# Kernel tuning notes

Measured on AMD Instinct MI355X. Metric: run time of the kernel, lower is better.

Reference implementation:

```python
import jax, jax.numpy as jnp
import numpy as np

N = 50000
E = 800000
IN = 256
H = 4
C = 64
HC = H * C
LAT = 64
EPS = 1e-5
NEG_SLOPE = 0.2


def setup_inputs() -> dict:
    key = jax.random.key(0)
    ks = jax.random.split(key, 20)
    g = lambda k, shape, fan: jax.random.normal(k, shape, jnp.float32) * (1.0 / np.sqrt(fan))
    return {
        "x": jax.random.normal(ks[0], (N, IN), jnp.float32),
        "edge_index": jax.random.randint(ks[1], (2, E), 0, N, jnp.int32),
        "Wl1": g(ks[2], (IN, HC), IN), "Wr1": g(ks[3], (IN, HC), IN),
        "att1": g(ks[4], (H, C), C), "b1": jnp.zeros((HC,), jnp.float32),
        "ln1_g": jnp.ones((HC,), jnp.float32), "ln1_b": jnp.zeros((HC,), jnp.float32),
        "Wl2": g(ks[5], (HC, HC), HC), "Wr2": g(ks[6], (HC, HC), HC),
        "att2": g(ks[7], (H, C), C), "b2": jnp.zeros((HC,), jnp.float32),
        "ln2_g": jnp.ones((HC,), jnp.float32), "ln2_b": jnp.zeros((HC,), jnp.float32),
        "Wmu": g(ks[8], (HC, LAT), HC), "bmu": jnp.zeros((LAT,), jnp.float32),
        "Wlv": g(ks[9], (HC, LAT), HC), "blv": jnp.zeros((LAT,), jnp.float32),
    }


def _gatv2_layer(x, src, dst, Wl, Wr, att, bias):
    # GATv2: e_ij = att . leaky_relu(Wl x_j + Wr x_i); segment softmax over dst; aggregate Wl x_j
    xl = (x @ Wl).reshape(-1, H, C)  # source transform [N,H,C]
    xr = (x @ Wr).reshape(-1, H, C)  # target transform [N,H,C]
    e = jax.nn.leaky_relu(xl[src] + xr[dst], NEG_SLOPE)   # [E',H,C]
    score = jnp.einsum('ehc,hc->eh', e, att)              # [E',H]
    m = jax.ops.segment_max(score, dst, num_segments=N)   # [N,H]
    ex = jnp.exp(score - m[dst])
    denom = jax.ops.segment_sum(ex, dst, num_segments=N)  # [N,H]
    alpha = ex / denom[dst]                               # self-loops guarantee denom > 0
    out = jax.ops.segment_sum(alpha[:, :, None] * xl[src], dst, num_segments=N)  # [N,H,C]
    return out.reshape(-1, HC) + bias


def _layernorm(x, g, b):
    mu = jnp.mean(x, axis=-1, keepdims=True)
    var = jnp.mean((x - mu) ** 2, axis=-1, keepdims=True)
    return (x - mu) * jax.lax.rsqrt(var + EPS) * g + b


def reference(x, edge_index, Wl1, Wr1, att1, b1, ln1_g, ln1_b,
              Wl2, Wr2, att2, b2, ln2_g, ln2_b, Wmu, bmu, Wlv, blv):
    loops = jnp.arange(N, dtype=edge_index.dtype)
    src = jnp.concatenate([edge_index[0], loops])  # add_self_loops=True
    dst = jnp.concatenate([edge_index[1], loops])
    h = _gatv2_layer(x, src, dst, Wl1, Wr1, att1, b1)
    h = jax.nn.elu(_layernorm(h, ln1_g, ln1_b))  # dropout is identity in eval mode
    h = _gatv2_layer(h, src, dst, Wl2, Wr2, att2, b2)
    h = jax.nn.elu(_layernorm(h, ln2_g, ln2_b))
    mu = h @ Wmu + bmu
    logvar = h @ Wlv + blv
    return mu, logvar
```

## Files before the change

### kernel.cpp

```cpp
#include <hip/hip_runtime.h>
#include <hip/hip_bf16.h>

#define NN 50000
#define NE 800000
#define HCn 256
#define LATn 64

typedef short bf16x4 __attribute__((ext_vector_type(4)));
typedef short bf16x8 __attribute__((ext_vector_type(8)));
typedef float f32x4 __attribute__((ext_vector_type(4)));

__device__ __forceinline__ short f2b(float f) {
    __hip_bfloat16 h = __float2bfloat16(f);
    return __builtin_bit_cast(short, h);
}
__device__ __forceinline__ float b2f(short s) {
    return __bfloat162float(__builtin_bit_cast(__hip_bfloat16, s));
}

#define SWZF(v, pat) __builtin_bit_cast(float, __builtin_amdgcn_ds_swizzle(__builtin_bit_cast(int, v), pat))

#define C04L2E 0.5770780163555854f
#define C06L2E 0.8656170245333781f
#define DEFER_THR 8.0f

__global__ void hist_kernel(const int* __restrict__ dst, int* __restrict__ counts) {
    int e = blockIdx.x * 256 + threadIdx.x;
    if (e < NE) atomicAdd(&counts[dst[e]], 1);
}

__global__ __launch_bounds__(1024) void scan1_kernel(int* __restrict__ counts,
                                                     int* __restrict__ blocksum) {
    const int g = blockIdx.x * 1024 + threadIdx.x;
    const int lane = threadIdx.x & 63;
    const int wv = threadIdx.x >> 6;
    int v = (g < NN) ? counts[g] : 0;
    int s = v;
#pragma unroll
    for (int d = 1; d < 64; d <<= 1) {
        int t = __shfl_up(s, d, 64);
        if (lane >= d) s += t;
    }
    __shared__ int wsum[16];
    if (lane == 63) wsum[wv] = s;
    __syncthreads();
    if (threadIdx.x == 0) {
        int run = 0;
#pragma unroll
        for (int q = 0; q < 16; ++q) { int t = wsum[q]; wsum[q] = run; run += t; }
        blocksum[blockIdx.x] = run;
    }
    __syncthreads();
    int excl = s - v + wsum[wv];
    if (g < NN) counts[g] = excl;
}

__global__ void scan2_kernel(int* __restrict__ blocksum, int* __restrict__ offsets, int nblk) {
    const int lane = threadIdx.x;
    int v = (lane < nblk) ? blocksum[lane] : 0;
    int s = v;
#pragma unroll
    for (int d = 1; d < 64; d <<= 1) {
        int t = __shfl_up(s, d, 64);
        if (lane >= d) s += t;
    }
    if (lane < nblk) blocksum[lane] = s - v;
    if (lane == 0) offsets[NN] = NE;
}

__global__ __launch_bounds__(1024) void scan3_kernel(const int* __restrict__ counts,
                                                     const int* __restrict__ blocksum,
                                                     int* __restrict__ offsets,
                                                     int* __restrict__ cursor) {
    const int g = blockIdx.x * 1024 + threadIdx.x;
    if (g < NN) {
        int v = counts[g] + blocksum[blockIdx.x];
        offsets[g] = v;
        cursor[g]  = v;
    }
}

__global__ void scatter_kernel(const int* __restrict__ src, const int* __restrict__ dst,
                               int* __restrict__ cursor, int* __restrict__ csr_src) {
    int e = blockIdx.x * 256 + threadIdx.x;
    if (e < NE) {
        int p = atomicAdd(&cursor[dst[e]], 1);
        csr_src[p] = src[e];
    }
}

__global__ __launch_bounds__(256) void cvt_x_kernel(const float* __restrict__ x,
                                                    short* __restrict__ xb) {
    long i = ((long)blockIdx.x * 256 + threadIdx.x) * 8;
    const f32x4* p = reinterpret_cast<const f32x4*>(x + i);
    f32x4 a = p[0], b = p[1];
    bf16x8 o;
#pragma unroll
    for (int j = 0; j < 4; ++j) { o[j] = f2b(a[j]); o[4 + j] = f2b(b[j]); }
    *reinterpret_cast<bf16x8*>(xb + i) = o;
}

__global__ void pack_w_kernel(const float* __restrict__ Wl1, const float* __restrict__ Wr1,
                              const float* __restrict__ Wl2, const float* __restrict__ Wr2,
                              const float* __restrict__ Wmu, const float* __restrict__ Wlv,
                              const float* __restrict__ bmu, const float* __restrict__ blv,
                              short* __restrict__ Wb1t, short* __restrict__ Wb2t,
                              short* __restrict__ Wb3t, float* __restrict__ bias3) {
    int i = blockIdx.x * 256 + threadIdx.x;
    const int S1 = 512 * 256, S2 = 2 * S1, S3 = S2 + 128 * 256;
    if (i < S1) {
        int c = i >> 8, k = i & 255;
        float v = (c < 256) ? Wl1[k * 256 + c] : Wr1[k * 256 + (c - 256)];
        Wb1t[i] = f2b(v);
    } else if (i < S2) {
        int j = i - S1; int c = j >> 8, k = j & 255;
        float v = (c < 256) ? Wl2[k * 256 + c] : Wr2[k * 256 + (c - 256)];
        Wb2t[j] = f2b(v);
    } else if (i < S3) {
        int j = i - S2; int c = j >> 8, k = j & 255;
        float v = (c < 64) ? Wmu[k * 64 + c] : Wlv[k * 64 + (c - 64)];
        Wb3t[j] = f2b(v);
    } else if (i < S3 + 128) {
        int c = i - S3;
        bias3[c] = (c < 64) ? bmu[c] : blv[c - 64];
    }
}

template<int OUT_MODE>
__global__ __launch_bounds__(256) void gemm_k(
    const short* __restrict__ A, const short* __restrict__ Wbt,
    void* __restrict__ outp, const float* __restrict__ bias, int Nc)
{
    __shared__ short Bs[64 * 264];
    const int t = threadIdx.x;
    const int w = t >> 6, lane = t & 63;
    const int row0 = blockIdx.x * 128, col0 = blockIdx.y * 64;

    {
        const int sn = t >> 2;
        const int sk0 = (t & 3) * 8;
        const short* wp = Wbt + (long)(col0 + sn) * 256 + sk0;
#pragma unroll
        for (int r = 0; r < 8; ++r) {
            int k = r * 32 + sk0;
            bf16x8 v = *reinterpret_cast<const bf16x8*>(wp + r * 32);
            *reinterpret_cast<bf16x8*>(&Bs[sn * 264 + k]) = v;
        }
    }
    __syncthreads();

    f32x4 acc[2][4];
#pragma unroll
    for (int a = 0; a < 2; ++a)
#pragma unroll
        for (int b = 0; b < 4; ++b) acc[a][b] = (f32x4){0.f, 0.f, 0.f, 0.f};

    const int arow = lane & 15, kq = lane >> 4;
    int r0 = row0 + w * 32 + arow;      if (r0 > NN - 1) r0 = NN - 1;
    int r1 = row0 + w * 32 + 16 + arow; if (r1 > NN - 1) r1 = NN - 1;
    const short* pa0 = A + (long)r0 * 256 + kq * 8;
    const short* pa1 = A + (long)r1 * 256 + kq * 8;

#pragma unroll
    for (int k0 = 0; k0 < 256; k0 += 32) {
        bf16x8 a0 = *reinterpret_cast<const bf16x8*>(pa0 + k0);
        bf16x8 a1 = *reinterpret_cast<const bf16x8*>(pa1 + k0);
#pragma unroll
        for (int nt = 0; nt < 4; ++nt) {
            bf16x8 b = *reinterpret_cast<const bf16x8*>(&Bs[(nt * 16 + arow) * 264 + k0 + kq * 8]);
            acc[0][nt] = __builtin_amdgcn_mfma_f32_16x16x32_bf16(a0, b, acc[0][nt], 0, 0, 0);
            acc[1][nt] = __builtin_amdgcn_mfma_f32_16x16x32_bf16(a1, b, acc[1][nt], 0, 0, 0);
        }
    }

#pragma unroll
    for (int rb = 0; rb < 2; ++rb)
#pragma unroll
        for (int nt = 0; nt < 4; ++nt) {
            int gcol = col0 + nt * 16 + arow;
#pragma unroll
            for (int r = 0; r < 4; ++r) {
                int grow = row0 + w * 32 + rb * 16 + kq * 4 + r;
                if (grow < NN) {
                    float v = acc[rb][nt][r];
                    if (OUT_MODE == 0) {
                        ((short*)outp)[(long)grow * Nc + gcol] = f2b(v);
                    } else {
                        v += bias[gcol];
                        float* o = (float*)outp;
                        if (gcol < 64) o[(long)grow * 64 + gcol] = v;
                        else           o[(long)NN * 64 + (long)grow * 64 + (gcol - 64)] = v;
                    }
                }
            }
        }
}

__global__ __launch_bounds__(256) void att_pre_kernel(
    const short* __restrict__ xlr, const float* __restrict__ att, float* __restrict__ a)
{
    const int i = blockIdx.x * 4 + (threadIdx.x >> 6);
    const int lane = threadIdx.x & 63;
    const int c4 = (lane >> 4) * 64 + (lane & 15) * 4;
    f32x4 attv = *reinterpret_cast<const f32x4*>(att + c4);
    bf16x4 v = *reinterpret_cast<const bf16x4*>(xlr + (long)i * 512 + c4);
    float s = 0.f;
#pragma unroll
    for (int k = 0; k < 4; ++k) s = fmaf(b2f(v[k]), attv[k], s);
    s += SWZF(s, 0x041F);
    s += SWZF(s, 0x081F);
    s += SWZF(s, 0x101F);
    s += SWZF(s, 0x201F);
    if ((lane & 15) == 0) a[i * 4 + (lane >> 4)] = s * C06L2E;
}

__device__ __forceinline__ void edge_abs_score(const short* __restrict__ xlr, int j, int c4,
                                               const float* xr, const f32x4& attv04,
                                               float* xf, float& s) {
    bf16x4 v = *reinterpret_cast<const bf16x4*>(xlr + (long)j * 512 + c4);
    s = 0.f;
#pragma unroll
    for (int k = 0; k < 4; ++k) {
        xf[k] = b2f(v[k]);
        float vv = xf[k] + xr[k];
        s = fmaf(attv04[k], fabsf(vv), s);
    }
    s += SWZF(s, 0x041F);
    s += SWZF(s, 0x081F);
    s += SWZF(s, 0x101F);
    s += SWZF(s, 0x201F);
}

__global__ __launch_bounds__(256) void gat_node_kernel(
    const short* __restrict__ xlr, const float* __restrict__ aarr,
    const int* __restrict__ offsets, const int* __restrict__ csr_src,
    const float* __restrict__ att, const float* __restrict__ bias,
    const float* __restrict__ ln_g, const float* __restrict__ ln_b,
    short* __restrict__ hout)
{
    const int i = blockIdx.x * 4 + (threadIdx.x >> 6);
    const int lane = threadIdx.x & 63;
    const int h  = lane >> 4;
    const int c4 = h * 64 + (lane & 15) * 4;

    f32x4 attv04 = *reinterpret_cast<const f32x4*>(att + c4);
#pragma unroll
    for (int k = 0; k < 4; ++k) attv04[k] *= C04L2E;

    float xr[4];
    {
        bf16x4 v = *reinterpret_cast<const bf16x4*>(xlr + (long)i * 512 + 256 + c4);
#pragma unroll
        for (int k = 0; k < 4; ++k) xr[k] = b2f(v[k]);
    }

    float m, l;
    float acc[4];
    {
        float aj = aarr[i * 4 + h];
        float xf[4], s;
        edge_abs_score(xlr, i, c4, xr, attv04, xf, s);
        m = s + aj; l = 1.f;
#pragma unroll
        for (int k = 0; k < 4; ++k) acc[k] = xf[k];
    }

    const int p0 = offsets[i], p1 = offsets[i + 1];
    int p = p0;
    for (; p + 4 <= p1; p += 4) {
        int jl = csr_src[p + (lane & 3)];
        int j0 = __builtin_amdgcn_readlane(jl, 0);
        int j1 = __builtin_amdgcn_readlane(jl, 1);
        int j2 = __builtin_amdgcn_readlane(jl, 2);
        int j3 = __builtin_amdgcn_readlane(jl, 3);
        float a0 = aarr[j0 * 4 + h], a1 = aarr[j1 * 4 + h];
        float a2 = aarr[j2 * 4 + h], a3 = aarr[j3 * 4 + h];
        float x0[4], x1[4], x2[4], x3[4], s0, s1, s2, s3;
        edge_abs_score(xlr, j0, c4, xr, attv04, x0, s0);
        edge_abs_score(xlr, j1, c4, xr, attv04, x1, s1);
        edge_abs_score(xlr, j2, c4, xr, attv04, x2, s2);
        edge_abs_score(xlr, j3, c4, xr, attv04, x3, s3);
        s0 += a0; s1 += a1; s2 += a2; s3 += a3;
        float sm = fmaxf(fmaxf(s0, s1), fmaxf(s2, s3));
        if (__all(sm <= m + DEFER_THR)) {
            float e0 = __builtin_amdgcn_exp2f(s0 - m);
            float e1 = __builtin_amdgcn_exp2f(s1 - m);
            float e2 = __builtin_amdgcn_exp2f(s2 - m);
            float e3 = __builtin_amdgcn_exp2f(s3 - m);
            l += (e0 + e1) + (e2 + e3);
#pragma unroll
            for (int k = 0; k < 4; ++k)
                acc[k] = fmaf(e0, x0[k], fmaf(e1, x1[k], fmaf(e2, x2[k], fmaf(e3, x3[k], acc[k]))));
        } else {
            float mn = fmaxf(m, sm);
            float corr = __builtin_amdgcn_exp2f(m - mn);
            float e0 = __builtin_amdgcn_exp2f(s0 - mn);
            float e1 = __builtin_amdgcn_exp2f(s1 - mn);
            float e2 = __builtin_amdgcn_exp2f(s2 - mn);
            float e3 = __builtin_amdgcn_exp2f(s3 - mn);
            l = fmaf(l, corr, (e0 + e1) + (e2 + e3));
#pragma unroll
            for (int k = 0; k < 4; ++k)
                acc[k] = fmaf(acc[k], corr,
                         fmaf(e0, x0[k], fmaf(e1, x1[k], fmaf(e2, x2[k], e3 * x3[k]))));
            m = mn;
        }
    }
    for (; p < p1; ++p) {
        int j = __builtin_amdgcn_readfirstlane(csr_src[p]);
        float aj = aarr[j * 4 + h];
        float xa[4], sa;
        edge_abs_score(xlr, j, c4, xr, attv04, xa, sa);
        sa += aj;
        if (__all(sa <= m + DEFER_THR)) {
            float ex = __builtin_amdgcn_exp2f(sa - m);
            l += ex;
#pragma unroll
            for (int k = 0; k < 4; ++k) acc[k] = fmaf(ex, xa[k], acc[k]);
        } else {
            float mn = fmaxf(m, sa);
            float corr = __builtin_amdgcn_exp2f(m - mn);
            float ex = __builtin_amdgcn_exp2f(sa - mn);
            l = fmaf(l, corr, ex);
#pragma unroll
            for (int k = 0; k < 4; ++k) acc[k] = fmaf(acc[k], corr, ex * xa[k]);
            m = mn;
        }
    }

    float inv = 1.f / l;
    f32x4 bv = *reinterpret_cast<const f32x4*>(bias + c4);
    float out[4], s1 = 0.f, s2 = 0.f;
#pragma unroll
    for (int k = 0; k < 4; ++k) {
        out[k] = acc[k] * inv + bv[k];
        s1 += out[k];
        s2 += out[k] * out[k];
    }
    s1 += SWZF(s1, 0x041F); s2 += SWZF(s2, 0x041F);
    s1 += SWZF(s1, 0x081F); s2 += SWZF(s2, 0x081F);
    s1 += SWZF(s1, 0x101F); s2 += SWZF(s2, 0x101F);
    s1 += SWZF(s1, 0x201F); s2 += SWZF(s2, 0x201F);
    s1 += SWZF(s1, 0x401F); s2 += SWZF(s2, 0x401F);
    s1 += __shfl_xor(s1, 32, 64);
    s2 += __shfl_xor(s2, 32, 64);
    float mu  = s1 * (1.f / 256.f);
    float var = s2 * (1.f / 256.f) - mu * mu;
    float rs  = rsqrtf(var + 1e-5f);
    f32x4 gv  = *reinterpret_cast<const f32x4*>(ln_g + c4);
    f32x4 bbv = *reinterpret_cast<const f32x4*>(ln_b + c4);
    bf16x4 o;
#pragma unroll
    for (int k = 0; k < 4; ++k) {
        float y = (out[k] - mu) * rs * gv[k] + bbv[k];
        y = y > 0.f ? y : expm1f(y);
        o[k] = f2b(y);
    }
    *reinterpret_cast<bf16x4*>(hout + (long)i * 256 + c4) = o;
}

extern "C" void kernel_launch(void* const* d_in, const int* in_sizes, int n_in,
                              void* d_out, int out_size, void* d_ws, size_t ws_size,
                              hipStream_t stream) {
    const float* x    = (const float*)d_in[0];
    const int*   ei   = (const int*)d_in[1];
    const float* Wl1  = (const float*)d_in[2];
    const float* Wr1  = (const float*)d_in[3];
    const float* att1 = (const float*)d_in[4];
    const float* b1   = (const float*)d_in[5];
    const float* ln1g = (const float*)d_in[6];
    const float* ln1b = (const float*)d_in[7];
    const float* Wl2  = (const float*)d_in[8];
    const float* Wr2  = (const float*)d_in[9];
    const float* att2 = (const float*)d_in[10];
    const float* b2   = (const float*)d_in[11];
    const float* ln2g = (const float*)d_in[12];
    const float* ln2b = (const float*)d_in[13];
    const float* Wmu  = (const float*)d_in[14];
    const float* bmu  = (const float*)d_in[15];
    const float* Wlv  = (const float*)d_in[16];
    const float* blv  = (const float*)d_in[17];

    short* bufXL = (short*)d_ws;
    short* bufH  = bufXL + (long)NN * 512;
    short* Wb1t  = bufH + (long)NN * 256;
    short* Wb2t  = Wb1t + 512 * 256;
    short* Wb3t  = Wb2t + 512 * 256;
    float* bias3 = (float*)(Wb3t + 128 * 256);
    int* counts  = (int*)(bias3 + 128);
    int* offsets = counts + NN;
    int* cursor  = offsets + NN + 1;
    int* csr_src = cursor + NN;
    int* blocksum = csr_src + NE;
    float* a_arr = (float*)(blocksum + 64);

    const int* src = ei;
    const int* dst = ei + NE;

    const int NBLK = (NN + 1023) / 1024;

    hipMemsetAsync(counts, 0, NN * sizeof(int), stream);
    hist_kernel<<<(NE + 255) / 256, 256, 0, stream>>>(dst, counts);
    scan1_kernel<<<NBLK, 1024, 0, stream>>>(counts, blocksum);
    scan2_kernel<<<1, 64, 0, stream>>>(blocksum, offsets, NBLK);
    scan3_kernel<<<NBLK, 1024, 0, stream>>>(counts, blocksum, offsets, cursor);
    scatter_kernel<<<(NE + 255) / 256, 256, 0, stream>>>(src, dst, cursor, csr_src);

    cvt_x_kernel<<<(NN * HCn) / (8 * 256), 256, 0, stream>>>(x, bufH);
    pack_w_kernel<<<1153, 256, 0, stream>>>(Wl1, Wr1, Wl2, Wr2, Wmu, Wlv, bmu, blv,
                                            Wb1t, Wb2t, Wb3t, bias3);

    const int GM = (NN + 127) / 128;
    dim3 g1(GM, 8);
    dim3 g3(GM, 2);

    gemm_k<0><<<g1, 256, 0, stream>>>(bufH, Wb1t, bufXL, nullptr, 512);
    att_pre_kernel<<<NN / 4, 256, 0, stream>>>(bufXL, att1, a_arr);
    gat_node_kernel<<<NN / 4, 256, 0, stream>>>(bufXL, a_arr, offsets, csr_src,
                                                att1, b1, ln1g, ln1b, bufH);
    gemm_k<0><<<g1, 256, 0, stream>>>(bufH, Wb2t, bufXL, nullptr, 512);
    att_pre_kernel<<<NN / 4, 256, 0, stream>>>(bufXL, att2, a_arr);
    gat_node_kernel<<<NN / 4, 256, 0, stream>>>(bufXL, a_arr, offsets, csr_src,
                                                att2, b2, ln2g, ln2b, bufH);
    gemm_k<1><<<g3, 256, 0, stream>>>(bufH, Wb3t, d_out, bias3, 128);
}
```

Baseline: 380.6 us.

## Process four edges per wave in parallel slots and widen GEMM column tile

After: 466.1 us. 1.22x slower.

```diff
diff --git a/kernel.cpp b/kernel.cpp
--- a/kernel.cpp
+++ b/kernel.cpp
@@ -131,31 +131,34 @@
     const short* __restrict__ A, const short* __restrict__ Wbt,
     void* __restrict__ outp, const float* __restrict__ bias, int Nc)
 {
-    __shared__ short Bs[64 * 264];
+    __shared__ short Bs[128 * 256];
     const int t = threadIdx.x;
     const int w = t >> 6, lane = t & 63;
-    const int row0 = blockIdx.x * 128, col0 = blockIdx.y * 64;
+    const int row0 = blockIdx.x * 128, col0 = blockIdx.y * 128;
 
     {
-        const int sn = t >> 2;
-        const int sk0 = (t & 3) * 8;
-        const short* wp = Wbt + (long)(col0 + sn) * 256 + sk0;
-#pragma unroll
-        for (int r = 0; r < 8; ++r) {
-            int k = r * 32 + sk0;
-            bf16x8 v = *reinterpret_cast<const bf16x8*>(wp + r * 32);
-            *reinterpret_cast<bf16x8*>(&Bs[sn * 264 + k]) = v;
+        const int sn = t >> 1;
+        const int half = t & 1;
+        const short* wp = Wbt + (long)(col0 + sn) * 256 + half * 128;
+        short* bp = &Bs[sn * 256];
+        const int sx = sn & 7;
+#pragma unroll
+        for (int r = 0; r < 16; ++r) {
+            bf16x8 v = *reinterpret_cast<const bf16x8*>(wp + r * 8);
+            int c = half * 16 + r;
+            *reinterpret_cast<bf16x8*>(bp + ((c ^ sx) * 8)) = v;
         }
     }
     __syncthreads();
 
-    f32x4 acc[2][4];
+    f32x4 acc[2][8];
 #pragma unroll
     for (int a = 0; a < 2; ++a)
 #pragma unroll
-        for (int b = 0; b < 4; ++b) acc[a][b] = (f32x4){0.f, 0.f, 0.f, 0.f};
+        for (int b = 0; b < 8; ++b) acc[a][b] = (f32x4){0.f, 0.f, 0.f, 0.f};
 
     const int arow = lane & 15, kq = lane >> 4;
+    const int xorc = arow & 7;
     int r0 = row0 + w * 32 + arow;      if (r0 > NN - 1) r0 = NN - 1;
     int r1 = row0 + w * 32 + 16 + arow; if (r1 > NN - 1) r1 = NN - 1;
     const short* pa0 = A + (long)r0 * 256 + kq * 8;
@@ -165,9 +168,11 @@
     for (int k0 = 0; k0 < 256; k0 += 32) {
         bf16x8 a0 = *reinterpret_cast<const bf16x8*>(pa0 + k0);
         bf16x8 a1 = *reinterpret_cast<const bf16x8*>(pa1 + k0);
-#pragma unroll
-        for (int nt = 0; nt < 4; ++nt) {
-            bf16x8 b = *reinterpret_cast<const bf16x8*>(&Bs[(nt * 16 + arow) * 264 + k0 + kq * 8]);
+        const int chunk = ((k0 >> 3) + kq) ^ xorc;
+        const short* bsp = &Bs[arow * 256 + chunk * 8];
+#pragma unroll
+        for (int nt = 0; nt < 8; ++nt) {
+            bf16x8 b = *reinterpret_cast<const bf16x8*>(bsp + nt * 4096);
             acc[0][nt] = __builtin_amdgcn_mfma_f32_16x16x32_bf16(a0, b, acc[0][nt], 0, 0, 0);
             acc[1][nt] = __builtin_amdgcn_mfma_f32_16x16x32_bf16(a1, b, acc[1][nt], 0, 0, 0);
         }
@@ -176,7 +181,7 @@
 #pragma unroll
     for (int rb = 0; rb < 2; ++rb)
 #pragma unroll
-        for (int nt = 0; nt < 4; ++nt) {
+        for (int nt = 0; nt < 8; ++nt) {
             int gcol = col0 + nt * 16 + arow;
 #pragma unroll
             for (int r = 0; r < 4; ++r) {
@@ -214,21 +219,27 @@
     if ((lane & 15) == 0) a[i * 4 + (lane >> 4)] = s * C06L2E;
 }
 
-__device__ __forceinline__ void edge_abs_score(const short* __restrict__ xlr, int j, int c4,
-                                               const float* xr, const f32x4& attv04,
-                                               float* xf, float& s) {
-    bf16x4 v = *reinterpret_cast<const bf16x4*>(xlr + (long)j * 512 + c4);
-    s = 0.f;
-#pragma unroll
-    for (int k = 0; k < 4; ++k) {
-        xf[k] = b2f(v[k]);
-        float vv = xf[k] + xr[k];
-        s = fmaf(attv04[k], fabsf(vv), s);
+__device__ __forceinline__ float edge16_score(const short* __restrict__ xlr, int j, int c16,
+                                              const float* xr, const float* attv, float* xf) {
+    const short* rp = xlr + (long)j * 512 + c16;
+    bf16x8 v0 = *reinterpret_cast<const bf16x8*>(rp);
+    bf16x8 v1 = *reinterpret_cast<const bf16x8*>(rp + 8);
+    float s = 0.f;
+#pragma unroll
+    for (int k = 0; k < 8; ++k) {
+        xf[k] = b2f(v0[k]);
+        float tv = xf[k] + xr[k];
+        s = fmaf(attv[k], fabsf(tv), s);
+    }
+#pragma unroll
+    for (int k = 0; k < 8; ++k) {
+        xf[8 + k] = b2f(v1[k]);
+        float tv = xf[8 + k] + xr[8 + k];
+        s = fmaf(attv[8 + k], fabsf(tv), s);
     }
     s += SWZF(s, 0x041F);
     s += SWZF(s, 0x081F);
-    s += SWZF(s, 0x101F);
-    s += SWZF(s, 0x201F);
+    return s;
 }
 
 __global__ __launch_bounds__(256) void gat_node_kernel(
@@ -240,123 +251,141 @@
 {
     const int i = blockIdx.x * 4 + (threadIdx.x >> 6);
     const int lane = threadIdx.x & 63;
-    const int h  = lane >> 4;
-    const int c4 = h * 64 + (lane & 15) * 4;
-
-    f32x4 attv04 = *reinterpret_cast<const f32x4*>(att + c4);
-#pragma unroll
-    for (int k = 0; k < 4; ++k) attv04[k] *= C04L2E;
-
-    float xr[4];
+    const int slot = lane >> 4;
+    const int il   = lane & 15;
+    const int h    = il >> 2;
+    const int c16  = h * 64 + (il & 3) * 16;
+
+    float attv[16], xr[16];
+#pragma unroll
+    for (int q = 0; q < 4; ++q) {
+        f32x4 tv = *reinterpret_cast<const f32x4*>(att + c16 + q * 4);
+#pragma unroll
+        for (int k = 0; k < 4; ++k) attv[q * 4 + k] = tv[k] * C04L2E;
+    }
     {
-        bf16x4 v = *reinterpret_cast<const bf16x4*>(xlr + (long)i * 512 + 256 + c4);
-#pragma unroll
-        for (int k = 0; k < 4; ++k) xr[k] = b2f(v[k]);
-    }
-
-    float m, l;
-    float acc[4];
+        const short* rp = xlr + (long)i * 512 + 256 + c16;
+        bf16x8 v0 = *reinterpret_cast<const bf16x8*>(rp);
+        bf16x8 v1 = *reinterpret_cast<const bf16x8*>(rp + 8);
+#pragma unroll
+        for (int k = 0; k < 8; ++k) { xr[k] = b2f(v0[k]); xr[8 + k] = b2f(v1[k]); }
+    }
+
+    const int p0 = offsets[i], p1 = offsets[i + 1];
+
+    float m, l, acc[16];
     {
-        float aj = aarr[i * 4 + h];
-        float xf[4], s;
-        edge_abs_score(xlr, i, c4, xr, attv04, xf, s);
-        m = s + aj; l = 1.f;
-#pragma unroll
-        for (int k = 0; k < 4; ++k) acc[k] = xf[k];
-    }
-
-    const int p0 = offsets[i], p1 = offsets[i + 1];
-    int p = p0;
+        int idx = p0 + slot - 1;
+        bool act = (slot == 0) || (idx < p1);
+        int j = i;
+        if (slot != 0 && act) j = csr_src[idx];
+        float xf[16];
+        float s = edge16_score(xlr, j, c16, xr, attv, xf) + aarr[j * 4 + h];
+        if (!act) s = -1e30f;
+        m = s; l = 1.f;
+#pragma unroll
+        for (int k = 0; k < 16; ++k) acc[k] = xf[k];
+    }
+
+    int p = p0 + 3;
     for (; p + 4 <= p1; p += 4) {
-        int jl = csr_src[p + (lane & 3)];
-        int j0 = __builtin_amdgcn_readlane(jl, 0);
-        int j1 = __builtin_amdgcn_readlane(jl, 1);
-        int j2 = __builtin_amdgcn_readlane(jl, 2);
-        int j3 = __builtin_amdgcn_readlane(jl, 3);
-        float a0 = aarr[j0 * 4 + h], a1 = aarr[j1 * 4 + h];
-        float a2 = aarr[j2 * 4 + h], a3 = aarr[j3 * 4 + h];
-        float x0[4], x1[4], x2[4], x3[4], s0, s1, s2, s3;
-        edge_abs_score(xlr, j0, c4, xr, attv04, x0, s0);
-        edge_abs_score(xlr, j1, c4, xr, attv04, x1, s1);
-        edge_abs_score(xlr, j2, c4, xr, attv04, x2, s2);
-        edge_abs_score(xlr, j3, c4, xr, attv04, x3, s3);
-        s0 += a0; s1 += a1; s2 += a2; s3 += a3;
-        float sm = fmaxf(fmaxf(s0, s1), fmaxf(s2, s3));
-        if (__all(sm <= m + DEFER_THR)) {
-            float e0 = __builtin_amdgcn_exp2f(s0 - m);
-            float e1 = __builtin_amdgcn_exp2f(s1 - m);
-            float e2 = __builtin_amdgcn_exp2f(s2 - m);
-            float e3 = __builtin_amdgcn_exp2f(s3 - m);
-            l += (e0 + e1) + (e2 + e3);
-#pragma unroll
-            for (int k = 0; k < 4; ++k)
-                acc[k] = fmaf(e0, x0[k], fmaf(e1, x1[k], fmaf(e2, x2[k], fmaf(e3, x3[k], acc[k]))));
+        int j = csr_src[p + slot];
+        float aj = aarr[j * 4 + h];
+        float xf[16];
+        float s = edge16_score(xlr, j, c16, xr, attv, xf) + aj;
+        if (__all(s <= m + DEFER_THR)) {
+            float e = __builtin_amdgcn_exp2f(s - m);
+            l += e;
+#pragma unroll
+            for (int k = 0; k < 16; ++k) acc[k] = fmaf(e, xf[k], acc[k]);
         } else {
-            float mn = fmaxf(m, sm);
+            float mn = fmaxf(m, s);
             float corr = __builtin_amdgcn_exp2f(m - mn);
-            float e0 = __builtin_amdgcn_exp2f(s0 - mn);
-            float e1 = __builtin_amdgcn_exp2f(s1 - mn);
-            float e2 = __builtin_amdgcn_exp2f(s2 - mn);
-            float e3 = __builtin_amdgcn_exp2f(s3 - mn);
-            l = fmaf(l, corr, (e0 + e1) + (e2 + e3));
-#pragma unroll
-            for (int k = 0; k < 4; ++k)
-                acc[k] = fmaf(acc[k], corr,
-                         fmaf(e0, x0[k], fmaf(e1, x1[k], fmaf(e2, x2[k], e3 * x3[k]))));
+            float e = __builtin_amdgcn_exp2f(s - mn);
+            l = fmaf(l, corr, e);
+#pragma unroll
+            for (int k = 0; k < 16; ++k) acc[k] = fmaf(acc[k], corr, e * xf[k]);
             m = mn;
         }
     }
-    for (; p < p1; ++p) {
-        int j = __builtin_amdgcn_readfirstlane(csr_src[p]);
+    if (p < p1) {
+        int idx = p + slot;
+        bool act = idx < p1;
+        int j = i;
+        if (act) j = csr_src[idx];
         float aj = aarr[j * 4 + h];
-        float xa[4], sa;
-        edge_abs_score(xlr, j, c4, xr, attv04, xa, sa);
-        sa += aj;
-        if (__all(sa <= m + DEFER_THR)) {
-            float ex = __builtin_amdgcn_exp2f(sa - m);
-            l += ex;
-#pragma unroll
-            for (int k = 0; k < 4; ++k) acc[k] = fmaf(ex, xa[k], acc[k]);
+        float xf[16];
+        float s = edge16_score(xlr, j, c16, xr, attv, xf) + aj;
+        if (!act) s = -1e30f;
+        if (__all(s <= m + DEFER_THR)) {
+            float e = __builtin_amdgcn_exp2f(s - m);
+            l += e;
+#pragma unroll
+            for (int k = 0; k < 16; ++k) acc[k] = fmaf(e, xf[k], acc[k]);
         } else {
-            float mn = fmaxf(m, sa);
+            float mn = fmaxf(m, s);
             float corr = __builtin_amdgcn_exp2f(m - mn);
-            float ex = __builtin_amdgcn_exp2f(sa - mn);
-            l = fmaf(l, corr, ex);
-#pragma unroll
-            for (int k = 0; k < 4; ++k) acc[k] = fmaf(acc[k], corr, ex * xa[k]);
+            float e = __builtin_amdgcn_exp2f(s - mn);
+            l = fmaf(l, corr, e);
+#pragma unroll
+            for (int k = 0; k < 16; ++k) acc[k] = fmaf(acc[k], corr, e * xf[k]);
             m = mn;
         }
     }
 
+    {
+        float mm = fmaxf(m, SWZF(m, 0x401F));
+        mm = fmaxf(mm, __shfl_xor(mm, 32, 64));
+        float f = __builtin_amdgcn_exp2f(m - mm);
+        l *= f;
+#pragma unroll
+        for (int k = 0; k < 16; ++k) acc[k] *= f;
+        l += SWZF(l, 0x401F);
+        l += __shfl_xor(l, 32, 64);
+#pragma unroll
+        for (int k = 0; k < 16; ++k) acc[k] += SWZF(acc[k], 0x401F);
+#pragma unroll
+        for (int k = 0; k < 16; ++k) acc[k] += __shfl_xor(acc[k], 32, 64);
+    }
+
     float inv = 1.f / l;
-    f32x4 bv = *reinterpret_cast<const f32x4*>(bias + c4);
-    float out[4], s1 = 0.f, s2 = 0.f;
-#pragma unroll
-    for (int k = 0; k < 4; ++k) {
-        out[k] = acc[k] * inv + bv[k];
-        s1 += out[k];
-        s2 += out[k] * out[k];
+    float out[16], s1 = 0.f, s2 = 0.f;
+#pragma unroll
+    for (int q = 0; q < 4; ++q) {
+        f32x4 bv = *reinterpret_cast<const f32x4*>(bias + c16 + q * 4);
+#pragma unroll
+        for (int k = 0; k < 4; ++k) {
+            float o = acc[q * 4 + k] * inv + bv[k];
+            out[q * 4 + k] = o;
+            s1 += o; s2 += o * o;
+        }
     }
     s1 += SWZF(s1, 0x041F); s2 += SWZF(s2, 0x041F);
     s1 += SWZF(s1, 0x081F); s2 += SWZF(s2, 0x081F);
     s1 += SWZF(s1, 0x101F); s2 += SWZF(s2, 0x101F);
     s1 += SWZF(s1, 0x201F); s2 += SWZF(s2, 0x201F);
-    s1 += SWZF(s1, 0x401F); s2 += SWZF(s2, 0x401F);
-    s1 += __shfl_xor(s1, 32, 64);
-    s2 += __shfl_xor(s2, 32, 64);
     float mu  = s1 * (1.f / 256.f);
     float var = s2 * (1.f / 256.f) - mu * mu;
     float rs  = rsqrtf(var + 1e-5f);
-    f32x4 gv  = *reinterpret_cast<const f32x4*>(ln_g + c4);
-    f32x4 bbv = *reinterpret_cast<const f32x4*>(ln_b + c4);
-    bf16x4 o;
-#pragma unroll
-    for (int k = 0; k < 4; ++k) {
-        float y = (out[k] - mu) * rs * gv[k] + bbv[k];
-        y = y > 0.f ? y : expm1f(y);
-        o[k] = f2b(y);
-    }
-    *reinterpret_cast<bf16x4*>(hout + (long)i * 256 + c4) = o;
+    bf16x8 o0, o1;
+#pragma unroll
+    for (int q = 0; q < 4; ++q) {
+        f32x4 gv  = *reinterpret_cast<const f32x4*>(ln_g + c16 + q * 4);
+        f32x4 bbv = *reinterpret_cast<const f32x4*>(ln_b + c16 + q * 4);
+#pragma unroll
+        for (int k = 0; k < 4; ++k) {
+            float y = (out[q * 4 + k] - mu) * rs * gv[k] + bbv[k];
+            y = y > 0.f ? y : expm1f(y);
+            short sb = f2b(y);
+            int kk = q * 4 + k;
+            if (kk < 8) o0[kk] = sb; else o1[kk - 8] = sb;
+        }
+    }
+    if (slot == 0) {
+        short* op = hout + (long)i * 256 + c16;
+        *reinterpret_cast<bf16x8*>(op)     = o0;
+        *reinterpret_cast<bf16x8*>(op + 8) = o1;
+    }
 }
 
 extern "C" void kernel_launch(void* const* d_in, const int* in_sizes, int n_in,
@@ -411,8 +440,8 @@
                                             Wb1t, Wb2t, Wb3t, bias3);
 
     const int GM = (NN + 127) / 128;
-    dim3 g1(GM, 8);
-    dim3 g3(GM, 2);
+    dim3 g1(GM, 4);
+    dim3 g3(GM, 1);
 
     gemm_k<0><<<g1, 256, 0, stream>>>(bufH, Wb1t, bufXL, nullptr, 512);
     att_pre_kernel<<<NN / 4, 256, 0, stream>>>(bufXL, att1, a_arr);
```
